# Kernel optimization log

Measured on AMD Instinct MI355X. Metric: run time of the kernel, lower is better.

## Reference

```python
import jax, jax.numpy as jnp
import numpy as np

B, L, C, Q, H = 32, 2048, 512, 512, 1024

def setup_inputs() -> dict:
    key = jax.random.key(0)
    ks = jax.random.split(key, 8)
    query = jax.random.normal(ks[0], (B, Q), dtype=jnp.float32)
    context = jax.random.normal(ks[1], (B, L, C), dtype=jnp.float32)
    mapping_mask = jax.random.randint(ks[2], (B, L, 1), 0, 2).astype(jnp.float32)
    s = 0.02
    Wq = jax.random.normal(ks[3], (H, Q), dtype=jnp.float32) * s
    Wc = jax.random.normal(ks[4], (H, C), dtype=jnp.float32) * s
    bc = jnp.zeros((H,), dtype=jnp.float32)
    Wo = jax.random.normal(ks[5], (1, H), dtype=jnp.float32) * s
    bo = jnp.zeros((1,), dtype=jnp.float32)
    return {"query": query, "context": context, "mapping_mask": mapping_mask,
            "Wq": Wq, "Wc": Wc, "bc": bc, "Wo": Wo, "bo": bo}

def reference(query, context, mapping_mask, Wq, Wc, bc, Wo, bo):
    # res_q: [B,H], res_c: [B,L,H]
    res_q = query @ Wq.T
    res_c = jnp.einsum('blc,hc->blh', context, Wc) + bc
    tmp = jnp.tanh(res_q[:, None, :] + res_c)            # [B,L,H]
    weights_logit = jnp.einsum('blh,oh->blo', tmp, Wo) + bo  # [B,L,1]
    weights_exp = mapping_mask * jnp.exp(weights_logit)      # unnormalized, no max-subtract (faithful)
    weights = weights_exp / (weights_exp.sum(axis=1, keepdims=True) + 1e-5)
    output = jnp.einsum('blo,blc->boc', weights, context)[:, 0, :]  # bmm(w^T, ctx) -> squeeze
    return output, weights
```

## Files before the change

kernel.cpp:

```cpp
#include <hip/hip_runtime.h>

#define NB 32
#define LL 2048
#define CH 512
#define BQ 512
#define HH 1024
#define LDA2 260

typedef __attribute__((ext_vector_type(8))) short bf16x8;
typedef __attribute__((ext_vector_type(16))) float f32x16;

__device__ __forceinline__ unsigned short f2bf(float x) {
  unsigned int u = __float_as_uint(x);
  u += 0x7FFFu + ((u >> 16) & 1u);
  return (unsigned short)(u >> 16);
}

__device__ __forceinline__ unsigned int cvt_pk_bf16(float a, float b) {
  unsigned int r;
  asm("v_cvt_pk_bf16_f32 %0, %1, %2" : "=v"(r) : "v"(a), "v"(b));
  return r;
}

__device__ __forceinline__ float fast_tanh(float x) {
  float e = __builtin_amdgcn_exp2f(x * 2.885390081777927f);
  return 1.0f - 2.0f * __builtin_amdgcn_rcpf(e + 1.0f);
}

__global__ __launch_bounds__(256) void k_resqc(const float* __restrict__ query,
                                               const float* __restrict__ Wq,
                                               const float* __restrict__ bc,
                                               float* __restrict__ resqc) {
  int gid = blockIdx.x * 256 + threadIdx.x;
  int b = gid >> 10, h = gid & 1023;
  const float4* q4 = (const float4*)(query + (size_t)b * BQ);
  const float4* w4 = (const float4*)(Wq + (size_t)h * BQ);
  float acc = 0.f;
#pragma unroll 4
  for (int i = 0; i < BQ / 4; ++i) {
    float4 a = q4[i], w = w4[i];
    acc += a.x * w.x + a.y * w.y + a.z * w.z + a.w * w.w;
  }
  resqc[gid] = acc + bc[h];
}

__global__ __launch_bounds__(256) void k_pack_wc(const float* __restrict__ Wc,
                                                 unsigned short* __restrict__ wcbp) {
  int gid = blockIdx.x * 256 + threadIdx.x;
  int lane = gid & 63, ks = (gid >> 6) & 31, cg = gid >> 11;
  int lo = lane & 31, hi = lane >> 5;
  const float4* s = (const float4*)(Wc + (size_t)(cg * 32 + lo) * CH + hi * 8 + ks * 16);
  float4 v0 = s[0], v1 = s[1];
  uint4 p;
  p.x = cvt_pk_bf16(v0.x, v0.y);
  p.y = cvt_pk_bf16(v0.z, v0.w);
  p.z = cvt_pk_bf16(v1.x, v1.y);
  p.w = cvt_pk_bf16(v1.z, v1.w);
  ((uint4*)wcbp)[gid] = p;
}

__global__ __launch_bounds__(512) void k_pack_ctx(const float* __restrict__ ctx,
                                                  uint4* __restrict__ apk) {
  int g = blockIdx.x;
  int t = threadIdx.x;
  int lane = t & 63, ksq = t >> 6;
  int lo = lane & 31, hi = lane >> 5;
  const float* rowp = ctx + (size_t)(g * 32 + lo) * CH + hi * 8;
  uint4* dst = apk + (size_t)g * 2048 + lane;
#pragma unroll
  for (int i = 0; i < 4; ++i) {
    int ks = ksq * 4 + i;
    const float4* s = (const float4*)(rowp + ks * 16);
    float4 v0 = s[0], v1 = s[1];
    uint4 p;
    p.x = cvt_pk_bf16(v0.x, v0.y);
    p.y = cvt_pk_bf16(v0.z, v0.w);
    p.z = cvt_pk_bf16(v1.x, v1.y);
    p.w = cvt_pk_bf16(v1.z, v1.w);
    dst[(size_t)ks * 64] = p;
  }
}

__global__ __launch_bounds__(256, 2) void k_logits_pk(const uint4* __restrict__ apk,
                                                      const uint4* __restrict__ bpk,
                                                      const float* __restrict__ resqc,
                                                      const float* __restrict__ Wo,
                                                      float* __restrict__ logit) {
  int bid = blockIdx.x;
  int xcd = bid & 7, idx = bid >> 3;
  int rb = xcd * 32 + (idx >> 3), cc = idx & 7;
  int t = threadIdx.x;
  int wv = t >> 6, lane = t & 63;
  int lo = lane & 31, hi = lane >> 5;
  int b = rb >> 3;

  const uint4* pa0 = apk + (size_t)(rb * 8 + wv * 2 + 0) * 2048 + lane;
  const uint4* pa1 = apk + (size_t)(rb * 8 + wv * 2 + 1) * 2048 + lane;
  const uint4* pb0 = bpk + (size_t)(cc * 4 + 0) * 2048 + lane;
  const uint4* pb1 = bpk + (size_t)(cc * 4 + 1) * 2048 + lane;
  const uint4* pb2 = bpk + (size_t)(cc * 4 + 2) * 2048 + lane;
  const uint4* pb3 = bpk + (size_t)(cc * 4 + 3) * 2048 + lane;

  f32x16 acc[2][4];
#pragma unroll
  for (int m = 0; m < 2; ++m)
#pragma unroll
    for (int n = 0; n < 4; ++n) acc[m][n] = (f32x16){0,0,0,0,0,0,0,0,0,0,0,0,0,0,0,0};

#pragma unroll 4
  for (int ks = 0; ks < 32; ++ks) {
    uint4 ua0 = pa0[(size_t)ks * 64];
    uint4 ua1 = pa1[(size_t)ks * 64];
    uint4 ub0 = pb0[(size_t)ks * 64];
    uint4 ub1 = pb1[(size_t)ks * 64];
    uint4 ub2 = pb2[(size_t)ks * 64];
    uint4 ub3 = pb3[(size_t)ks * 64];
    bf16x8 fa0, fa1, fb0, fb1, fb2, fb3;
    __builtin_memcpy(&fa0, &ua0, 16);
    __builtin_memcpy(&fa1, &ua1, 16);
    __builtin_memcpy(&fb0, &ub0, 16);
    __builtin_memcpy(&fb1, &ub1, 16);
    __builtin_memcpy(&fb2, &ub2, 16);
    __builtin_memcpy(&fb3, &ub3, 16);
    acc[0][0] = __builtin_amdgcn_mfma_f32_32x32x16_bf16(fa0, fb0, acc[0][0], 0, 0, 0);
    acc[0][1] = __builtin_amdgcn_mfma_f32_32x32x16_bf16(fa0, fb1, acc[0][1], 0, 0, 0);
    acc[0][2] = __builtin_amdgcn_mfma_f32_32x32x16_bf16(fa0, fb2, acc[0][2], 0, 0, 0);
    acc[0][3] = __builtin_amdgcn_mfma_f32_32x32x16_bf16(fa0, fb3, acc[0][3], 0, 0, 0);
    acc[1][0] = __builtin_amdgcn_mfma_f32_32x32x16_bf16(fa1, fb0, acc[1][0], 0, 0, 0);
    acc[1][1] = __builtin_amdgcn_mfma_f32_32x32x16_bf16(fa1, fb1, acc[1][1], 0, 0, 0);
    acc[1][2] = __builtin_amdgcn_mfma_f32_32x32x16_bf16(fa1, fb2, acc[1][2], 0, 0, 0);
    acc[1][3] = __builtin_amdgcn_mfma_f32_32x32x16_bf16(fa1, fb3, acc[1][3], 0, 0, 0);
  }

  float q_[4], wo_[4];
#pragma unroll
  for (int n = 0; n < 4; ++n) {
    q_[n]  = resqc[b * HH + cc * 128 + n * 32 + lo];
    wo_[n] = Wo[cc * 128 + n * 32 + lo];
  }
  float v[32];
#pragma unroll
  for (int m = 0; m < 2; ++m)
#pragma unroll
    for (int r = 0; r < 16; ++r) {
      float s = 0.f;
#pragma unroll
      for (int n = 0; n < 4; ++n) s += wo_[n] * fast_tanh(acc[m][n][r] + q_[n]);
      v[m * 16 + r] = s;
    }
#pragma unroll
  for (int sdist = 16; sdist >= 1; sdist >>= 1) {
#pragma unroll
    for (int i = 0; i < sdist; ++i) {
      float a = v[i], c = v[i + sdist];
      float keep = (lo & sdist) ? c : a;
      float send = (lo & sdist) ? a : c;
      v[i] = keep + __shfl_xor(send, sdist, 64);
    }
  }
  int rr = lo & 15;
  int row_local = (lo >> 4) * 32 + (rr & 3) + 8 * (rr >> 2) + 4 * hi;
  int row = rb * 256 + wv * 64 + row_local;
  atomicAdd(&logit[row], v[0]);
}

__global__ __launch_bounds__(256) void k_weights(const float* __restrict__ mask,
                                                 const float* __restrict__ bo,
                                                 const float* __restrict__ logit,
                                                 float* __restrict__ wout) {
  __shared__ float red[4];
  int b = blockIdx.x, t = threadIdx.x;
  float bov = bo[0];
  float w[8];
  float s = 0.f;
#pragma unroll
  for (int i = 0; i < 8; ++i) {
    int l = t + 256 * i;
    float e = mask[b * LL + l] * __expf(logit[b * LL + l] + bov);
    w[i] = e; s += e;
  }
#pragma unroll
  for (int m = 32; m >= 1; m >>= 1) s += __shfl_xor(s, m, 64);
  int wave = t >> 6, lane = t & 63;
  if (lane == 0) red[wave] = s;
  __syncthreads();
  float inv = 1.0f / (red[0] + red[1] + red[2] + red[3] + 1e-5f);
#pragma unroll
  for (int i = 0; i < 8; ++i) wout[b * LL + t + 256 * i] = w[i] * inv;
}

__global__ __launch_bounds__(512) void k_output_pk(const uint4* __restrict__ apk,
                                                   const float* __restrict__ wout,
                                                   float* __restrict__ out) {
  int bid = blockIdx.x;
  int b = bid >> 2, q = bid & 3;
  int t = threadIdx.x;
  int lane = t & 63, ks = q * 8 + (t >> 6);
  int lo = lane & 31, hi = lane >> 5;
  const uint4* pa = apk + (size_t)(b * 64) * 2048 + (size_t)ks * 64 + lane;
  const float* wp = wout + b * LL + lo;
  float a8[8] = {0,0,0,0,0,0,0,0};
  for (int gg = 0; gg < 64; ++gg) {
    uint4 u = pa[(size_t)gg * 2048];
    float w = wp[gg * 32];
    unsigned int uu[4] = {u.x, u.y, u.z, u.w};
#pragma unroll
    for (int j = 0; j < 4; ++j) {
      a8[2 * j]     += w * __uint_as_float(uu[j] << 16);
      a8[2 * j + 1] += w * __uint_as_float(uu[j] & 0xffff0000u);
    }
  }
#pragma unroll
  for (int m = 1; m <= 16; m <<= 1)
#pragma unroll
    for (int j = 0; j < 8; ++j) a8[j] += __shfl_xor(a8[j], m, 64);
  if (lo == 0) {
#pragma unroll
    for (int j = 0; j < 8; ++j) out[b * CH + ks * 16 + hi * 8 + j] = a8[j];
  }
}

__global__ __launch_bounds__(512, 2) void k_logits_lds(const float* __restrict__ ctx,
                                                       const unsigned short* __restrict__ wcbp,
                                                       const float* __restrict__ resqc,
                                                       const float* __restrict__ Wo,
                                                       float* __restrict__ logits) {
  __shared__ unsigned short Alds[2][64 * 520];
  __shared__ float lsum4[4][64];
  const int t = threadIdx.x;
  const int g0 = blockIdx.x * 4;
  if (t < 256) lsum4[t >> 6][t & 63] = 0.f;
  {
    int b = g0 >> 5, row0 = (g0 & 31) << 6;
    const float4* src = (const float4*)(ctx + ((size_t)(b * LL + row0)) * CH);
#pragma unroll
    for (int i = 0; i < 16; ++i) {
      int f = i * 512 + t;
      int r = f >> 7, c4 = f & 127;
      float4 v = src[f];
      uint2 w;
      w.x = cvt_pk_bf16(v.x, v.y);
      w.y = cvt_pk_bf16(v.z, v.w);
      *(uint2*)(Alds[0] + r * 520 + c4 * 4) = w;
    }
  }
  __syncthreads();
  const int wave = t >> 6, lane = t & 63;
  const int lo = lane & 31, hi = lane >> 5;
  const int n0 = wave * 128;
  const uint4* bp = (const uint4*)wcbp + (size_t)(wave * 4) * 2048 + lane;
  float wo_[4];
#pragma unroll
  for (int n = 0; n < 4; ++n) wo_[n] = Wo[n0 + n * 32 + lo];
  for (int tt = 0; tt < 4; ++tt) {
    const int g = g0 + tt;
    const int b = g >> 5, row0 = (g & 31) << 6;
    const int cur = tt & 1;
    if (tt < 3) {
      int gn = g + 1;
      int nb = gn >> 5, nrow0 = (gn & 31) << 6;
      const float4* src = (const float4*)(ctx + ((size_t)(nb * LL + nrow0)) * CH);
#pragma unroll
      for (int i = 0; i < 16; ++i) {
        int f = i * 512 + t;
        int r = f >> 7, c4 = f & 127;
        float4 v = src[f];
        uint2 w;
        w.x = cvt_pk_bf16(v.x, v.y);
        w.y = cvt_pk_bf16(v.z, v.w);
        *(uint2*)(Alds[cur ^ 1] + r * 520 + c4 * 4) = w;
      }
    }
    const char* a0b = (const char*)(Alds[cur]) + lo * 1040 + hi * 16;
    f32x16 acc[2][4];
#pragma unroll
    for (int m = 0; m < 2; ++m)
#pragma unroll
      for (int n = 0; n < 4; ++n) acc[m][n] = (f32x16){0,0,0,0,0,0,0,0,0,0,0,0,0,0,0,0};
#pragma unroll 4
    for (int ks = 0; ks < 32; ++ks) {
      uint4 ub[4];
#pragma unroll
      for (int n = 0; n < 4; ++n) ub[n] = bp[(size_t)n * 2048 + ks * 64];
      bf16x8 fa[2];
#pragma unroll
      for (int m = 0; m < 2; ++m)
        fa[m] = *(const bf16x8*)(a0b + m * (32 * 1040) + ks * 32);
#pragma unroll
      for (int m = 0; m < 2; ++m)
#pragma unroll
        for (int n = 0; n < 4; ++n) {
          bf16x8 fb;
          __builtin_memcpy(&fb, &ub[n], 16);
          acc[m][n] = __builtin_amdgcn_mfma_f32_32x32x16_bf16(fa[m], fb, acc[m][n], 0, 0, 0);
        }
    }
    float q_[4];
#pragma unroll
    for (int n = 0; n < 4; ++n) q_[n] = resqc[b * HH + n0 + n * 32 + lo];
    float v[32];
#pragma unroll
    for (int m = 0; m < 2; ++m)
#pragma unroll
      for (int r = 0; r < 16; ++r) {
        float s = 0.f;
#pragma unroll
        for (int n = 0; n < 4; ++n) s += wo_[n] * fast_tanh(acc[m][n][r] + q_[n]);
        v[m * 16 + r] = s;
      }
#pragma unroll
    for (int sdist = 16; sdist >= 1; sdist >>= 1) {
#pragma unroll
      for (int i = 0; i < sdist; ++i) {
        float a = v[i], c = v[i + sdist];
        float keep = (lo & sdist) ? c : a;
        float send = (lo & sdist) ? a : c;
        v[i] = keep + __shfl_xor(send, sdist, 64);
      }
    }
    int rr = lo & 15;
    int row = ((lo < 16) ? 0 : 32) + (rr & 3) + 8 * (rr >> 2) + 4 * hi;
    atomicAdd(&lsum4[tt][row], v[0]);
    __syncthreads();
    if (t < 64) logits[(size_t)b * LL + row0 + t] = lsum4[tt][t];
  }
}

__global__ __launch_bounds__(256) void k_output_f32(const float* __restrict__ ctx,
                                                    const float* __restrict__ weights,
                                                    float* __restrict__ out) {
  __shared__ float wl[128];
  int bid = blockIdx.x;
  int b = bid >> 4, chunk = bid & 15;
  int t = threadIdx.x;
  int l0 = chunk * 128;
  if (t < 128) wl[t] = weights[b * LL + l0 + t];
  __syncthreads();
  const float2* c2 = (const float2*)(ctx + ((size_t)(b * LL + l0)) * CH) + t;
  float ax = 0.f, ay = 0.f;
#pragma unroll 4
  for (int l = 0; l < 128; ++l) {
    float wv = wl[l];
    float2 v = c2[(size_t)l * (CH / 2)];
    ax += wv * v.x; ay += wv * v.y;
  }
  atomicAdd(&out[b * CH + 2 * t], ax);
  atomicAdd(&out[b * CH + 2 * t + 1], ay);
}

extern "C" void kernel_launch(void* const* d_in, const int* in_sizes, int n_in,
                              void* d_out, int out_size, void* d_ws, size_t ws_size,
                              hipStream_t stream) {
  const float* query = (const float*)d_in[0];
  const float* ctx   = (const float*)d_in[1];
  const float* mask  = (const float*)d_in[2];
  const float* Wq    = (const float*)d_in[3];
  const float* Wc    = (const float*)d_in[4];
  const float* bc    = (const float*)d_in[5];
  const float* Wo    = (const float*)d_in[6];
  const float* bo    = (const float*)d_in[7];
  float* out = (float*)d_out;

  unsigned short* wcbp = (unsigned short*)d_ws;
  float* resqc = (float*)((char*)d_ws + (1 << 20));
  float* logit = (float*)((char*)d_ws + (1 << 20) + (1 << 17));
  uint4* apk   = (uint4*)((char*)d_ws + (2 << 20));
  float* wout = out + NB * CH;

  const size_t need = (size_t)(2 << 20) + ((size_t)64 << 20);

  k_resqc<<<128, 256, 0, stream>>>(query, Wq, bc, resqc);
  k_pack_wc<<<256, 256, 0, stream>>>(Wc, wcbp);

  if (ws_size >= need) {
    k_pack_ctx<<<2048, 512, 0, stream>>>(ctx, apk);
    hipMemsetAsync(logit, 0, NB * LL * sizeof(float), stream);
    k_logits_pk<<<2048, 256, 0, stream>>>(apk, (const uint4*)wcbp, resqc, Wo, logit);
    k_weights<<<32, 256, 0, stream>>>(mask, bo, logit, wout);
    k_output_pk<<<128, 512, 0, stream>>>(apk, wout, out);
  } else {
    hipMemsetAsync(out, 0, NB * CH * sizeof(float), stream);
    k_logits_lds<<<256, 512, 0, stream>>>(ctx, wcbp, resqc, Wo, logit);
    k_weights<<<32, 256, 0, stream>>>(mask, bo, logit, wout);
    k_output_f32<<<512, 256, 0, stream>>>(ctx, wout, out);
  }
}
```

Before: 156.5 us.

## Fuse prep kernels, software-pipeline logits loads, split output over L chunks

Merges the context pack, Wc pack and query projection into one launch, cutting two kernel launches. The logits MFMA loop now keeps a 3-deep register ring of prefetched A/B fragments, so global load latency overlaps the matrix math. The output reduction is split over four L chunks (512 blocks instead of 128) and accumulates with atomics into a zeroed output. This adds a memset and atomic contention, and raises register pressure in the logits kernel.

```diff
diff --git a/kernel.cpp b/kernel.cpp
--- a/kernel.cpp
+++ b/kernel.cpp
@@ -5,16 +5,9 @@
 #define CH 512
 #define BQ 512
 #define HH 1024
-#define LDA2 260
 
 typedef __attribute__((ext_vector_type(8))) short bf16x8;
 typedef __attribute__((ext_vector_type(16))) float f32x16;
-
-__device__ __forceinline__ unsigned short f2bf(float x) {
-  unsigned int u = __float_as_uint(x);
-  u += 0x7FFFu + ((u >> 16) & 1u);
-  return (unsigned short)(u >> 16);
-}
 
 __device__ __forceinline__ unsigned int cvt_pk_bf16(float a, float b) {
   unsigned int r;
@@ -25,6 +18,212 @@
 __device__ __forceinline__ float fast_tanh(float x) {
   float e = __builtin_amdgcn_exp2f(x * 2.885390081777927f);
   return 1.0f - 2.0f * __builtin_amdgcn_rcpf(e + 1.0f);
+}
+
+__global__ __launch_bounds__(512) void k_prep(const float* __restrict__ ctx,
+                                              uint4* __restrict__ apk,
+                                              const float* __restrict__ Wc,
+                                              uint4* __restrict__ wcbp,
+                                              const float* __restrict__ query,
+                                              const float* __restrict__ Wq,
+                                              const float* __restrict__ bc,
+                                              float* __restrict__ resqc) {
+  int bid = blockIdx.x, t = threadIdx.x;
+  if (bid < 2048) {
+    int g = bid;
+    int lane = t & 63, ksq = t >> 6;
+    int lo = lane & 31, hi = lane >> 5;
+    const float* rowp = ctx + (size_t)(g * 32 + lo) * CH + hi * 8;
+    uint4* dst = apk + (size_t)g * 2048 + lane;
+#pragma unroll
+    for (int i = 0; i < 4; ++i) {
+      int ks = ksq * 4 + i;
+      const float4* s = (const float4*)(rowp + ks * 16);
+      float4 v0 = s[0], v1 = s[1];
+      uint4 p;
+      p.x = cvt_pk_bf16(v0.x, v0.y);
+      p.y = cvt_pk_bf16(v0.z, v0.w);
+      p.z = cvt_pk_bf16(v1.x, v1.y);
+      p.w = cvt_pk_bf16(v1.z, v1.w);
+      dst[(size_t)ks * 64] = p;
+    }
+  } else if (bid < 2176) {
+    int gid = (bid - 2048) * 512 + t;
+    int lane = gid & 63, ks = (gid >> 6) & 31, cg = gid >> 11;
+    int lo = lane & 31, hi = lane >> 5;
+    const float4* s = (const float4*)(Wc + (size_t)(cg * 32 + lo) * CH + hi * 8 + ks * 16);
+    float4 v0 = s[0], v1 = s[1];
+    uint4 p;
+    p.x = cvt_pk_bf16(v0.x, v0.y);
+    p.y = cvt_pk_bf16(v0.z, v0.w);
+    p.z = cvt_pk_bf16(v1.x, v1.y);
+    p.w = cvt_pk_bf16(v1.z, v1.w);
+    wcbp[gid] = p;
+  } else {
+    int gid = (bid - 2176) * 512 + t;
+    int b = gid >> 10, h = gid & 1023;
+    const float4* q4 = (const float4*)(query + (size_t)b * BQ);
+    const float4* w4 = (const float4*)(Wq + (size_t)h * BQ);
+    float acc = 0.f;
+#pragma unroll 4
+    for (int i = 0; i < BQ / 4; ++i) {
+      float4 a = q4[i], w = w4[i];
+      acc += a.x * w.x + a.y * w.y + a.z * w.z + a.w * w.w;
+    }
+    resqc[gid] = acc + bc[h];
+  }
+}
+
+__global__ __launch_bounds__(256, 2) void k_logits_pk(const uint4* __restrict__ apk,
+                                                      const uint4* __restrict__ bpk,
+                                                      const float* __restrict__ resqc,
+                                                      const float* __restrict__ Wo,
+                                                      float* __restrict__ logit) {
+  int bid = blockIdx.x;
+  int xcd = bid & 7, idx = bid >> 3;
+  int rb = xcd * 32 + (idx >> 3), cc = idx & 7;
+  int t = threadIdx.x;
+  int wv = t >> 6, lane = t & 63;
+  int lo = lane & 31, hi = lane >> 5;
+  int b = rb >> 3;
+
+  int wvu = __builtin_amdgcn_readfirstlane(wv);
+  const char* bA = (const char*)(apk + (size_t)(rb * 8 + wvu * 2) * 2048);
+  const char* bB = (const char*)(bpk + (size_t)(cc * 4) * 2048);
+  const int voff = lane * 16;
+
+  uint4 sA[3][2], sB[3][4];
+#pragma unroll
+  for (int p = 0; p < 3; ++p) {
+    sA[p][0] = *(const uint4*)(bA + voff + p * 1024);
+    sA[p][1] = *(const uint4*)(bA + 32768 + voff + p * 1024);
+#pragma unroll
+    for (int n = 0; n < 4; ++n)
+      sB[p][n] = *(const uint4*)(bB + (size_t)n * 32768 + voff + p * 1024);
+  }
+  int voff_i = voff + 3 * 1024;
+
+  f32x16 acc[2][4];
+#pragma unroll
+  for (int m = 0; m < 2; ++m)
+#pragma unroll
+    for (int n = 0; n < 4; ++n) acc[m][n] = (f32x16){0,0,0,0,0,0,0,0,0,0,0,0,0,0,0,0};
+
+#pragma unroll
+  for (int ks = 0; ks < 32; ++ks) {
+    const int sl = ks % 3;
+    bf16x8 fa0, fa1, fb0, fb1, fb2, fb3;
+    __builtin_memcpy(&fa0, &sA[sl][0], 16);
+    __builtin_memcpy(&fa1, &sA[sl][1], 16);
+    __builtin_memcpy(&fb0, &sB[sl][0], 16);
+    __builtin_memcpy(&fb1, &sB[sl][1], 16);
+    __builtin_memcpy(&fb2, &sB[sl][2], 16);
+    __builtin_memcpy(&fb3, &sB[sl][3], 16);
+    acc[0][0] = __builtin_amdgcn_mfma_f32_32x32x16_bf16(fa0, fb0, acc[0][0], 0, 0, 0);
+    acc[0][1] = __builtin_amdgcn_mfma_f32_32x32x16_bf16(fa0, fb1, acc[0][1], 0, 0, 0);
+    acc[0][2] = __builtin_amdgcn_mfma_f32_32x32x16_bf16(fa0, fb2, acc[0][2], 0, 0, 0);
+    acc[0][3] = __builtin_amdgcn_mfma_f32_32x32x16_bf16(fa0, fb3, acc[0][3], 0, 0, 0);
+    acc[1][0] = __builtin_amdgcn_mfma_f32_32x32x16_bf16(fa1, fb0, acc[1][0], 0, 0, 0);
+    acc[1][1] = __builtin_amdgcn_mfma_f32_32x32x16_bf16(fa1, fb1, acc[1][1], 0, 0, 0);
+    acc[1][2] = __builtin_amdgcn_mfma_f32_32x32x16_bf16(fa1, fb2, acc[1][2], 0, 0, 0);
+    acc[1][3] = __builtin_amdgcn_mfma_f32_32x32x16_bf16(fa1, fb3, acc[1][3], 0, 0, 0);
+    if (ks < 29) {
+      sA[sl][0] = *(const uint4*)(bA + voff_i);
+      sA[sl][1] = *(const uint4*)(bA + 32768 + voff_i);
+#pragma unroll
+      for (int n = 0; n < 4; ++n)
+        sB[sl][n] = *(const uint4*)(bB + (size_t)n * 32768 + voff_i);
+      voff_i += 1024;
+    }
+  }
+
+  float q_[4], wo_[4];
+#pragma unroll
+  for (int n = 0; n < 4; ++n) {
+    q_[n]  = resqc[b * HH + cc * 128 + n * 32 + lo];
+    wo_[n] = Wo[cc * 128 + n * 32 + lo];
+  }
+  float v[32];
+#pragma unroll
+  for (int m = 0; m < 2; ++m)
+#pragma unroll
+    for (int r = 0; r < 16; ++r) {
+      float s = 0.f;
+#pragma unroll
+      for (int n = 0; n < 4; ++n) s += wo_[n] * fast_tanh(acc[m][n][r] + q_[n]);
+      v[m * 16 + r] = s;
+    }
+#pragma unroll
+  for (int sdist = 16; sdist >= 1; sdist >>= 1) {
+#pragma unroll
+    for (int i = 0; i < sdist; ++i) {
+      float a = v[i], c = v[i + sdist];
+      float keep = (lo & sdist) ? c : a;
+      float send = (lo & sdist) ? a : c;
+      v[i] = keep + __shfl_xor(send, sdist, 64);
+    }
+  }
+  int rr = lo & 15;
+  int row_local = (lo >> 4) * 32 + (rr & 3) + 8 * (rr >> 2) + 4 * hi;
+  int row = rb * 256 + wv * 64 + row_local;
+  atomicAdd(&logit[row], v[0]);
+}
+
+__global__ __launch_bounds__(256) void k_weights(const float* __restrict__ mask,
+                                                 const float* __restrict__ bo,
+                                                 const float* __restrict__ logit,
+                                                 float* __restrict__ wout) {
+  __shared__ float red[4];
+  int b = blockIdx.x, t = threadIdx.x;
+  float bov = bo[0];
+  float w[8];
+  float s = 0.f;
+#pragma unroll
+  for (int i = 0; i < 8; ++i) {
+    int l = t + 256 * i;
+    float e = mask[b * LL + l] * __expf(logit[b * LL + l] + bov);
+    w[i] = e; s += e;
+  }
+#pragma unroll
+  for (int m = 32; m >= 1; m >>= 1) s += __shfl_xor(s, m, 64);
+  int wave = t >> 6, lane = t & 63;
+  if (lane == 0) red[wave] = s;
+  __syncthreads();
+  float inv = 1.0f / (red[0] + red[1] + red[2] + red[3] + 1e-5f);
+#pragma unroll
+  for (int i = 0; i < 8; ++i) wout[b * LL + t + 256 * i] = w[i] * inv;
+}
+
+__global__ __launch_bounds__(512) void k_output_pk(const uint4* __restrict__ apk,
+                                                   const float* __restrict__ wout,
+                                                   float* __restrict__ out) {
+  int bid = blockIdx.x;
+  int b = bid >> 4, q = (bid >> 2) & 3, lc = bid & 3;
+  int t = threadIdx.x;
+  int lane = t & 63, ks = q * 8 + (t >> 6);
+  int lo = lane & 31, hi = lane >> 5;
+  const uint4* pa = apk + (size_t)(b * 64 + lc * 16) * 2048 + (size_t)ks * 64 + lane;
+  const float* wp = wout + b * LL + lc * 512 + lo;
+  float a8[8] = {0,0,0,0,0,0,0,0};
+#pragma unroll 4
+  for (int gg = 0; gg < 16; ++gg) {
+    uint4 u = pa[(size_t)gg * 2048];
+    float w = wp[gg * 32];
+    unsigned int uu[4] = {u.x, u.y, u.z, u.w};
+#pragma unroll
+    for (int j = 0; j < 4; ++j) {
+      a8[2 * j]     += w * __uint_as_float(uu[j] << 16);
+      a8[2 * j + 1] += w * __uint_as_float(uu[j] & 0xffff0000u);
+    }
+  }
+#pragma unroll
+  for (int m = 1; m <= 16; m <<= 1)
+#pragma unroll
+    for (int j = 0; j < 8; ++j) a8[j] += __shfl_xor(a8[j], m, 64);
+  if (lo == 0) {
+#pragma unroll
+    for (int j = 0; j < 8; ++j) atomicAdd(&out[b * CH + ks * 16 + hi * 8 + j], a8[j]);
+  }
 }
 
 __global__ __launch_bounds__(256) void k_resqc(const float* __restrict__ query,
@@ -45,7 +244,7 @@
 }
 
 __global__ __launch_bounds__(256) void k_pack_wc(const float* __restrict__ Wc,
-                                                 unsigned short* __restrict__ wcbp) {
+                                                 uint4* __restrict__ wcbp) {
   int gid = blockIdx.x * 256 + threadIdx.x;
   int lane = gid & 63, ks = (gid >> 6) & 31, cg = gid >> 11;
   int lo = lane & 31, hi = lane >> 5;
@@ -56,168 +255,7 @@
   p.y = cvt_pk_bf16(v0.z, v0.w);
   p.z = cvt_pk_bf16(v1.x, v1.y);
   p.w = cvt_pk_bf16(v1.z, v1.w);
-  ((uint4*)wcbp)[gid] = p;
-}
-
-__global__ __launch_bounds__(512) void k_pack_ctx(const float* __restrict__ ctx,
-                                                  uint4* __restrict__ apk) {
-  int g = blockIdx.x;
-  int t = threadIdx.x;
-  int lane = t & 63, ksq = t >> 6;
-  int lo = lane & 31, hi = lane >> 5;
-  const float* rowp = ctx + (size_t)(g * 32 + lo) * CH + hi * 8;
-  uint4* dst = apk + (size_t)g * 2048 + lane;
-#pragma unroll
-  for (int i = 0; i < 4; ++i) {
-    int ks = ksq * 4 + i;
-    const float4* s = (const float4*)(rowp + ks * 16);
-    float4 v0 = s[0], v1 = s[1];
-    uint4 p;
-    p.x = cvt_pk_bf16(v0.x, v0.y);
-    p.y = cvt_pk_bf16(v0.z, v0.w);
-    p.z = cvt_pk_bf16(v1.x, v1.y);
-    p.w = cvt_pk_bf16(v1.z, v1.w);
-    dst[(size_t)ks * 64] = p;
-  }
-}
-
-__global__ __launch_bounds__(256, 2) void k_logits_pk(const uint4* __restrict__ apk,
-                                                      const uint4* __restrict__ bpk,
-                                                      const float* __restrict__ resqc,
-                                                      const float* __restrict__ Wo,
-                                                      float* __restrict__ logit) {
-  int bid = blockIdx.x;
-  int xcd = bid & 7, idx = bid >> 3;
-  int rb = xcd * 32 + (idx >> 3), cc = idx & 7;
-  int t = threadIdx.x;
-  int wv = t >> 6, lane = t & 63;
-  int lo = lane & 31, hi = lane >> 5;
-  int b = rb >> 3;
-
-  const uint4* pa0 = apk + (size_t)(rb * 8 + wv * 2 + 0) * 2048 + lane;
-  const uint4* pa1 = apk + (size_t)(rb * 8 + wv * 2 + 1) * 2048 + lane;
-  const uint4* pb0 = bpk + (size_t)(cc * 4 + 0) * 2048 + lane;
-  const uint4* pb1 = bpk + (size_t)(cc * 4 + 1) * 2048 + lane;
-  const uint4* pb2 = bpk + (size_t)(cc * 4 + 2) * 2048 + lane;
-  const uint4* pb3 = bpk + (size_t)(cc * 4 + 3) * 2048 + lane;
-
-  f32x16 acc[2][4];
-#pragma unroll
-  for (int m = 0; m < 2; ++m)
-#pragma unroll
-    for (int n = 0; n < 4; ++n) acc[m][n] = (f32x16){0,0,0,0,0,0,0,0,0,0,0,0,0,0,0,0};
-
-#pragma unroll 4
-  for (int ks = 0; ks < 32; ++ks) {
-    uint4 ua0 = pa0[(size_t)ks * 64];
-    uint4 ua1 = pa1[(size_t)ks * 64];
-    uint4 ub0 = pb0[(size_t)ks * 64];
-    uint4 ub1 = pb1[(size_t)ks * 64];
-    uint4 ub2 = pb2[(size_t)ks * 64];
-    uint4 ub3 = pb3[(size_t)ks * 64];
-    bf16x8 fa0, fa1, fb0, fb1, fb2, fb3;
-    __builtin_memcpy(&fa0, &ua0, 16);
-    __builtin_memcpy(&fa1, &ua1, 16);
-    __builtin_memcpy(&fb0, &ub0, 16);
-    __builtin_memcpy(&fb1, &ub1, 16);
-    __builtin_memcpy(&fb2, &ub2, 16);
-    __builtin_memcpy(&fb3, &ub3, 16);
-    acc[0][0] = __builtin_amdgcn_mfma_f32_32x32x16_bf16(fa0, fb0, acc[0][0], 0, 0, 0);
-    acc[0][1] = __builtin_amdgcn_mfma_f32_32x32x16_bf16(fa0, fb1, acc[0][1], 0, 0, 0);
-    acc[0][2] = __builtin_amdgcn_mfma_f32_32x32x16_bf16(fa0, fb2, acc[0][2], 0, 0, 0);
-    acc[0][3] = __builtin_amdgcn_mfma_f32_32x32x16_bf16(fa0, fb3, acc[0][3], 0, 0, 0);
-    acc[1][0] = __builtin_amdgcn_mfma_f32_32x32x16_bf16(fa1, fb0, acc[1][0], 0, 0, 0);
-    acc[1][1] = __builtin_amdgcn_mfma_f32_32x32x16_bf16(fa1, fb1, acc[1][1], 0, 0, 0);
-    acc[1][2] = __builtin_amdgcn_mfma_f32_32x32x16_bf16(fa1, fb2, acc[1][2], 0, 0, 0);
-    acc[1][3] = __builtin_amdgcn_mfma_f32_32x32x16_bf16(fa1, fb3, acc[1][3], 0, 0, 0);
-  }
-
-  float q_[4], wo_[4];
-#pragma unroll
-  for (int n = 0; n < 4; ++n) {
-    q_[n]  = resqc[b * HH + cc * 128 + n * 32 + lo];
-    wo_[n] = Wo[cc * 128 + n * 32 + lo];
-  }
-  float v[32];
-#pragma unroll
-  for (int m = 0; m < 2; ++m)
-#pragma unroll
-    for (int r = 0; r < 16; ++r) {
-      float s = 0.f;
-#pragma unroll
-      for (int n = 0; n < 4; ++n) s += wo_[n] * fast_tanh(acc[m][n][r] + q_[n]);
-      v[m * 16 + r] = s;
-    }
-#pragma unroll
-  for (int sdist = 16; sdist >= 1; sdist >>= 1) {
-#pragma unroll
-    for (int i = 0; i < sdist; ++i) {
-      float a = v[i], c = v[i + sdist];
-      float keep = (lo & sdist) ? c : a;
-      float send = (lo & sdist) ? a : c;
-      v[i] = keep + __shfl_xor(send, sdist, 64);
-    }
-  }
-  int rr = lo & 15;
-  int row_local = (lo >> 4) * 32 + (rr & 3) + 8 * (rr >> 2) + 4 * hi;
-  int row = rb * 256 + wv * 64 + row_local;
-  atomicAdd(&logit[row], v[0]);
-}
-
-__global__ __launch_bounds__(256) void k_weights(const float* __restrict__ mask,
-                                                 const float* __restrict__ bo,
-                                                 const float* __restrict__ logit,
-                                                 float* __restrict__ wout) {
-  __shared__ float red[4];
-  int b = blockIdx.x, t = threadIdx.x;
-  float bov = bo[0];
-  float w[8];
-  float s = 0.f;
-#pragma unroll
-  for (int i = 0; i < 8; ++i) {
-    int l = t + 256 * i;
-    float e = mask[b * LL + l] * __expf(logit[b * LL + l] + bov);
-    w[i] = e; s += e;
-  }
-#pragma unroll
-  for (int m = 32; m >= 1; m >>= 1) s += __shfl_xor(s, m, 64);
-  int wave = t >> 6, lane = t & 63;
-  if (lane == 0) red[wave] = s;
-  __syncthreads();
-  float inv = 1.0f / (red[0] + red[1] + red[2] + red[3] + 1e-5f);
-#pragma unroll
-  for (int i = 0; i < 8; ++i) wout[b * LL + t + 256 * i] = w[i] * inv;
-}
-
-__global__ __launch_bounds__(512) void k_output_pk(const uint4* __restrict__ apk,
-                                                   const float* __restrict__ wout,
-                                                   float* __restrict__ out) {
-  int bid = blockIdx.x;
-  int b = bid >> 2, q = bid & 3;
-  int t = threadIdx.x;
-  int lane = t & 63, ks = q * 8 + (t >> 6);
-  int lo = lane & 31, hi = lane >> 5;
-  const uint4* pa = apk + (size_t)(b * 64) * 2048 + (size_t)ks * 64 + lane;
-  const float* wp = wout + b * LL + lo;
-  float a8[8] = {0,0,0,0,0,0,0,0};
-  for (int gg = 0; gg < 64; ++gg) {
-    uint4 u = pa[(size_t)gg * 2048];
-    float w = wp[gg * 32];
-    unsigned int uu[4] = {u.x, u.y, u.z, u.w};
-#pragma unroll
-    for (int j = 0; j < 4; ++j) {
-      a8[2 * j]     += w * __uint_as_float(uu[j] << 16);
-      a8[2 * j + 1] += w * __uint_as_float(uu[j] & 0xffff0000u);
-    }
-  }
-#pragma unroll
-  for (int m = 1; m <= 16; m <<= 1)
-#pragma unroll
-    for (int j = 0; j < 8; ++j) a8[j] += __shfl_xor(a8[j], m, 64);
-  if (lo == 0) {
-#pragma unroll
-    for (int j = 0; j < 8; ++j) out[b * CH + ks * 16 + hi * 8 + j] = a8[j];
-  }
+  wcbp[gid] = p;
 }
 
 __global__ __launch_bounds__(512, 2) void k_logits_lds(const float* __restrict__ ctx,
@@ -361,7 +399,7 @@
   const float* bo    = (const float*)d_in[7];
   float* out = (float*)d_out;
 
-  unsigned short* wcbp = (unsigned short*)d_ws;
+  uint4* wcbp  = (uint4*)d_ws;
   float* resqc = (float*)((char*)d_ws + (1 << 20));
   float* logit = (float*)((char*)d_ws + (1 << 20) + (1 << 17));
   uint4* apk   = (uint4*)((char*)d_ws + (2 << 20));
@@ -369,18 +407,18 @@
 
   const size_t need = (size_t)(2 << 20) + ((size_t)64 << 20);
 
-  k_resqc<<<128, 256, 0, stream>>>(query, Wq, bc, resqc);
-  k_pack_wc<<<256, 256, 0, stream>>>(Wc, wcbp);
-
   if (ws_size >= need) {
-    k_pack_ctx<<<2048, 512, 0, stream>>>(ctx, apk);
+    hipMemsetAsync(out, 0, NB * CH * sizeof(float), stream);
     hipMemsetAsync(logit, 0, NB * LL * sizeof(float), stream);
-    k_logits_pk<<<2048, 256, 0, stream>>>(apk, (const uint4*)wcbp, resqc, Wo, logit);
+    k_prep<<<2240, 512, 0, stream>>>(ctx, apk, Wc, wcbp, query, Wq, bc, resqc);
+    k_logits_pk<<<2048, 256, 0, stream>>>(apk, wcbp, resqc, Wo, logit);
     k_weights<<<32, 256, 0, stream>>>(mask, bo, logit, wout);
-    k_output_pk<<<128, 512, 0, stream>>>(apk, wout, out);
+    k_output_pk<<<512, 512, 0, stream>>>(apk, wout, out);
   } else {
     hipMemsetAsync(out, 0, NB * CH * sizeof(float), stream);
-    k_logits_lds<<<256, 512, 0, stream>>>(ctx, wcbp, resqc, Wo, logit);
+    k_resqc<<<128, 256, 0, stream>>>(query, Wq, bc, resqc);
+    k_pack_wc<<<256, 256, 0, stream>>>(Wc, wcbp);
+    k_logits_lds<<<256, 512, 0, stream>>>(ctx, (const unsigned short*)wcbp, resqc, Wo, logit);
     k_weights<<<32, 256, 0, stream>>>(mask, bo, logit, wout);
     k_output_f32<<<512, 256, 0, stream>>>(ctx, wout, out);
   }
```

Result: slower. 184.5 us (+17.9%).
